# Kernel tuning notes

Measured on AMD Instinct MI355X. Metric: run time of the kernel, lower is better.

The kernel has to match this reference:

```python
import jax, jax.numpy as jnp
import numpy as np

B, U, D, N, O = 128, 16, 256, 1024, 256
RES_CONN, IN_CONN, BIAS_P = 0.2, 0.2, 0.5


def _fixed_bernoulli(rng, heads, rows, cols, conn):
    # each column has exactly nb = int(conn*rows) ones (as in the torch code)
    nb = max(1, int(conn * rows))
    r = rng.random((heads, rows, cols))
    thr = np.sort(r, axis=1)[:, nb - 1:nb, :]
    return (r <= thr).astype(np.float32)


def setup_inputs() -> dict:
    rng = np.random.default_rng(0)
    # recurrent weights: normal * fixed-bernoulli mask, normalized by spectral radius
    W = rng.normal(size=(U, N, N)).astype(np.float32) * _fixed_bernoulli(rng, U, N, N, RES_CONN)
    sr0 = np.abs(np.linalg.eigvals(W.astype(np.float64))).max(axis=-1).astype(np.float32).reshape(U, 1, 1)
    W = W / sr0
    Win = _fixed_bernoulli(rng, U, D, N, IN_CONN)
    bias = (rng.random((U, 1, N)) < BIAS_P).astype(np.float32)
    Wout = rng.normal(size=(U, N, O)).astype(np.float32)
    adaptive_lr = rng.random((U, D, 1)).astype(np.float32)
    sr = rng.random((U, 1, 1)).astype(np.float32)
    temperature = np.ones((1,), np.float32)
    X = rng.normal(size=(B, U, D)).astype(np.float32)
    state = rng.normal(size=(B, U, N)).astype(np.float32)
    arrs = dict(X=X, state=state, W=W, Win=Win, bias=bias, Wout=Wout,
                sr=sr, adaptive_lr=adaptive_lr, temperature=temperature)
    return {k: jnp.asarray(v) for k, v in arrs.items()}


def reference(X, state, W, Win, bias, Wout, sr, adaptive_lr, temperature):
    # X: [B,U,D] -> [B,U,1,D]; state: [B,U,N] -> [B,U,1,N]
    x = X[:, :, None, :]
    s = state[:, :, None, :]
    # adaptive per-unit learning rate: softmax over the units axis
    lr = jax.nn.softmax(jnp.einsum('buid,udk->buik', x, adaptive_lr) / temperature, axis=1)  # [B,U,1,1]
    feed = jnp.einsum('buid,udn->buin', x, Win)            # [B,U,1,N]
    echo = jnp.einsum('buin,unm->buim', s, W * sr) + bias  # [B,U,1,N]
    new_state = (1.0 - lr) * s + lr * jnp.tanh(feed + echo)
    output = jnp.einsum('buin,uno->buio', new_state, Wout)  # [B,U,1,O]
    return new_state[:, :, 0, :], output[:, :, 0, :]
```

## Files before the change

kernel.cpp:

```cpp
#include <hip/hip_runtime.h>
#include <math.h>

#define Bsz 128
#define Usz 16
#define Dsz 256
#define Nsz 1024
#define Osz 256

typedef __attribute__((ext_vector_type(4))) float f32x4;
typedef __attribute__((ext_vector_type(8))) short bf16x8;
typedef __attribute__((ext_vector_type(4))) unsigned int u32x4;

union cell_u { u32x4 u; bf16x8 b; };

struct F8 { f32x4 lo, hi; };

__device__ __forceinline__ unsigned int fbits(float f) {
    union { float f; unsigned int u; } v; v.f = f; return v.u;
}
__device__ __forceinline__ unsigned int pk(float lo, float hi) {
    return __builtin_amdgcn_perm(fbits(hi), fbits(lo), 0x07060302u);
}
__device__ __forceinline__ bf16x8 pkF8(F8 f, float s) {
    f.lo *= s; f.hi *= s;
    cell_u r;
    r.u[0] = pk(f.lo[0], f.lo[1]); r.u[1] = pk(f.lo[2], f.lo[3]);
    r.u[2] = pk(f.hi[0], f.hi[1]); r.u[3] = pk(f.hi[2], f.hi[3]);
    return r.b;
}
__device__ __forceinline__ F8 ld8c(const float* p) {
    F8 r; r.lo = *(const f32x4*)p; r.hi = *(const f32x4*)(p + 4); return r;
}
__device__ __forceinline__ F8 ld8s(const float* p, int str) {
    F8 r;
    r.lo[0] = p[0];              r.lo[1] = p[(size_t)str];
    r.lo[2] = p[2 * (size_t)str]; r.lo[3] = p[3 * (size_t)str];
    r.hi[0] = p[4 * (size_t)str]; r.hi[1] = p[5 * (size_t)str];
    r.hi[2] = p[6 * (size_t)str]; r.hi[3] = p[7 * (size_t)str];
    return r;
}

__global__ __launch_bounds__(256)
void lr_kernel(const float* __restrict__ X, const float* __restrict__ alr,
               const float* __restrict__ temp, float* __restrict__ lr)
{
    const int b = blockIdx.x;
    const int t = threadIdx.x;
    const int u = t >> 4;
    const int l = t & 15;
    const float* xp = X + ((size_t)b * Usz + u) * Dsz;
    const float* ap = alr + (size_t)u * Dsz;
    float s = 0.f;
    for (int d = l; d < Dsz; d += 16) s += xp[d] * ap[d];
    s += __shfl_down(s, 8, 16);
    s += __shfl_down(s, 4, 16);
    s += __shfl_down(s, 2, 16);
    s += __shfl_down(s, 1, 16);
    __shared__ float logits[16];
    if (l == 0) logits[u] = s;
    __syncthreads();
    if (t < 16) {
        const float T = temp[0];
        float m = -1e30f;
        #pragma unroll
        for (int i = 0; i < 16; i++) m = fmaxf(m, logits[i] / T);
        float sum = 0.f;
        #pragma unroll
        for (int i = 0; i < 16; i++) sum += expf(logits[i] / T - m);
        lr[(size_t)b * Usz + t] = expf(logits[t] / T - m) / sum;
    }
}

struct Step { F8 a0, a1, b0, b1; };

__global__ __launch_bounds__(256)
void state_mfma(const float* __restrict__ X, const float* __restrict__ state,
                const float* __restrict__ W, const float* __restrict__ Win,
                const float* __restrict__ bias, const float* __restrict__ sr,
                const float* __restrict__ lr, float* __restrict__ out0)
{
    const int id = blockIdx.x;
    const int u  = id & 15;
    const int nt = (id >> 4) & 15;
    const int mt = id >> 8;

    const int tid  = threadIdx.x;
    const int wave = tid >> 6, lane = tid & 63;
    const int l16  = lane & 15, kgl = lane >> 4;
    const int wm = wave & 1, wn = wave >> 1;

    const int row0 = mt * 64 + wm * 32 + l16;
    const int col0 = nt * 64 + wn * 32 + l16;

    const float sru = sr[u];

    const float* Ax0 = X + ((size_t)row0 * Usz + u) * Dsz;
    const float* Ax1 = X + ((size_t)(row0 + 16) * Usz + u) * Dsz;
    const float* Ae0 = state + ((size_t)row0 * Usz + u) * Nsz;
    const float* Ae1 = state + ((size_t)(row0 + 16) * Usz + u) * Nsz;
    const float* Bf  = Win + (size_t)u * Dsz * Nsz + col0;
    const float* Be  = W   + (size_t)u * Nsz * Nsz + col0;

    f32x4 acc[2][2] = {};

    auto ldS = [&](int s) -> Step {
        const int kb = s * 32 + kgl * 8;
        Step st;
        if (kb < Dsz) {
            st.a0 = ld8c(Ax0 + kb);
            st.a1 = ld8c(Ax1 + kb);
            const float* pb = Bf + (size_t)kb * Nsz;
            st.b0 = ld8s(pb, Nsz);
            st.b1 = ld8s(pb + 16, Nsz);
        } else {
            const int kk = kb - Dsz;
            st.a0 = ld8c(Ae0 + kk);
            st.a1 = ld8c(Ae1 + kk);
            const float* pb = Be + (size_t)kk * Nsz;
            st.b0 = ld8s(pb, Nsz);
            st.b1 = ld8s(pb + 16, Nsz);
        }
        return st;
    };
    auto compute = [&](Step st, int s) {
        const float asc = (s < 8) ? 1.f : sru;
        const bf16x8 af0 = pkF8(st.a0, asc), af1 = pkF8(st.a1, asc);
        const bf16x8 bf0 = pkF8(st.b0, 1.f), bf1 = pkF8(st.b1, 1.f);
        acc[0][0] = __builtin_amdgcn_mfma_f32_16x16x32_bf16(af0, bf0, acc[0][0], 0, 0, 0);
        acc[0][1] = __builtin_amdgcn_mfma_f32_16x16x32_bf16(af0, bf1, acc[0][1], 0, 0, 0);
        acc[1][0] = __builtin_amdgcn_mfma_f32_16x16x32_bf16(af1, bf0, acc[1][0], 0, 0, 0);
        acc[1][1] = __builtin_amdgcn_mfma_f32_16x16x32_bf16(af1, bf1, acc[1][1], 0, 0, 0);
    };

    Step sa = ldS(0);
    for (int s = 0; s < 40; s += 2) {
        Step sb = ldS(s + 1);
        compute(sa, s);
        if (s + 2 < 40) sa = ldS(s + 2);
        compute(sb, s + 1);
    }

    #pragma unroll
    for (int ni = 0; ni < 2; ni++) {
        const int gcol = nt * 64 + wn * 32 + ni * 16 + l16;
        const float bi = bias[u * Nsz + gcol];
        #pragma unroll
        for (int mi = 0; mi < 2; mi++) {
            #pragma unroll
            for (int rg = 0; rg < 4; rg++) {
                const int grow = mt * 64 + wm * 32 + mi * 16 + kgl * 4 + rg;
                const size_t idx = ((size_t)grow * Usz + u) * Nsz + gcol;
                const float th = tanhf(acc[mi][ni][rg] + bi);
                const float sv = state[idx];
                const float lv = lr[grow * Usz + u];
                out0[idx] = (1.f - lv) * sv + lv * th;
            }
        }
    }
}

__global__ __launch_bounds__(256)
void out_mfma(const float* __restrict__ ns, const float* __restrict__ Wout,
              float* __restrict__ out1)
{
    const int w  = blockIdx.x * 4 + (threadIdx.x >> 6);
    const int u  = w & 15;
    const int ot = (w >> 4) & 15;
    const int mtw = w >> 8;

    const int lane = threadIdx.x & 63;
    const int l16  = lane & 15, kgl = lane >> 4;

    const float* Ap = ns + ((size_t)(mtw * 16 + l16) * Usz + u) * Nsz;
    const float* Bp = Wout + (size_t)u * Nsz * Osz + ot * 16 + l16;

    f32x4 acc = {};

    struct Step2 { F8 a, b; };
    auto ldS = [&](int s) -> Step2 {
        const int kb = s * 32 + kgl * 8;
        Step2 st;
        st.a = ld8c(Ap + kb);
        st.b = ld8s(Bp + (size_t)kb * Osz, Osz);
        return st;
    };
    auto compute = [&](Step2 st) {
        const bf16x8 af = pkF8(st.a, 1.f);
        const bf16x8 bf = pkF8(st.b, 1.f);
        acc = __builtin_amdgcn_mfma_f32_16x16x32_bf16(af, bf, acc, 0, 0, 0);
    };

    Step2 sa = ldS(0);
    for (int s = 0; s < 32; s += 2) {
        Step2 sb = ldS(s + 1);
        compute(sa);
        if (s + 2 < 32) sa = ldS(s + 2);
        compute(sb);
    }

    const int gcol = ot * 16 + l16;
    #pragma unroll
    for (int rg = 0; rg < 4; rg++) {
        const int grow = mtw * 16 + kgl * 4 + rg;
        out1[((size_t)grow * Usz + u) * Osz + gcol] = acc[rg];
    }
}

extern "C" void kernel_launch(void* const* d_in, const int* in_sizes, int n_in,
                              void* d_out, int out_size, void* d_ws, size_t ws_size,
                              hipStream_t stream)
{
    (void)in_sizes; (void)n_in; (void)out_size; (void)ws_size;
    const float* X     = (const float*)d_in[0];
    const float* state = (const float*)d_in[1];
    const float* W     = (const float*)d_in[2];
    const float* Win   = (const float*)d_in[3];
    const float* bias  = (const float*)d_in[4];
    const float* Wout  = (const float*)d_in[5];
    const float* sr    = (const float*)d_in[6];
    const float* alr   = (const float*)d_in[7];
    const float* temp  = (const float*)d_in[8];

    float* out0 = (float*)d_out;
    float* out1 = out0 + (size_t)Bsz * Usz * Nsz;
    float* lr   = (float*)d_ws;

    lr_kernel<<<Bsz, 256, 0, stream>>>(X, alr, temp, lr);
    state_mfma<<<512, 256, 0, stream>>>(X, state, W, Win, bias, sr, lr, out0);
    out_mfma<<<512, 256, 0, stream>>>(out0, Wout, out1);
}
```

Measured before the change: 216.7 us.

## Split-K both GEMMs across four slices with separate reduction kernels

Both batched GEMMs are split along K into four slices. Each slice writes partial sums to a workspace, and separate reduce kernels add the partials and apply bias, tanh and the leaky update (or just the sum for the output GEMM). This raises the grid from 512 to 2048 blocks so more CUs stay busy, at the cost of extra global traffic for partials and two more launches. The manual software-pipelined prefetch was also removed, and the old path is kept as a fallback when the workspace is too small.

```diff
diff --git a/kernel.cpp b/kernel.cpp
--- a/kernel.cpp
+++ b/kernel.cpp
@@ -33,7 +33,7 @@
 }
 __device__ __forceinline__ F8 ld8s(const float* p, int str) {
     F8 r;
-    r.lo[0] = p[0];              r.lo[1] = p[(size_t)str];
+    r.lo[0] = p[0];               r.lo[1] = p[(size_t)str];
     r.lo[2] = p[2 * (size_t)str]; r.lo[3] = p[3 * (size_t)str];
     r.hi[0] = p[4 * (size_t)str]; r.hi[1] = p[5 * (size_t)str];
     r.hi[2] = p[6 * (size_t)str]; r.hi[3] = p[7 * (size_t)str];
@@ -71,18 +71,16 @@
     }
 }
 
-struct Step { F8 a0, a1, b0, b1; };
-
-__global__ __launch_bounds__(256)
-void state_mfma(const float* __restrict__ X, const float* __restrict__ state,
-                const float* __restrict__ W, const float* __restrict__ Win,
-                const float* __restrict__ bias, const float* __restrict__ sr,
-                const float* __restrict__ lr, float* __restrict__ out0)
+__global__ __launch_bounds__(256)
+void state_split(const float* __restrict__ X, const float* __restrict__ state,
+                 const float* __restrict__ W, const float* __restrict__ Win,
+                 const float* __restrict__ sr, float* __restrict__ part)
 {
     const int id = blockIdx.x;
     const int u  = id & 15;
     const int nt = (id >> 4) & 15;
-    const int mt = id >> 8;
+    const int mt = (id >> 8) & 1;
+    const int ks = id >> 9;
 
     const int tid  = threadIdx.x;
     const int wave = tid >> 6, lane = tid & 63;
@@ -91,6 +89,7 @@
 
     const int row0 = mt * 64 + wm * 32 + l16;
     const int col0 = nt * 64 + wn * 32 + l16;
+    const int k0   = ks * 320;
 
     const float sru = sr[u];
 
@@ -103,43 +102,180 @@
 
     f32x4 acc[2][2] = {};
 
-    auto ldS = [&](int s) -> Step {
-        const int kb = s * 32 + kgl * 8;
-        Step st;
+    for (int s = 0; s < 10; ++s) {
+        const int kb = k0 + s * 32 + kgl * 8;
+        F8 a0, a1, b0, b1;
         if (kb < Dsz) {
-            st.a0 = ld8c(Ax0 + kb);
-            st.a1 = ld8c(Ax1 + kb);
+            a0 = ld8c(Ax0 + kb);
+            a1 = ld8c(Ax1 + kb);
             const float* pb = Bf + (size_t)kb * Nsz;
-            st.b0 = ld8s(pb, Nsz);
-            st.b1 = ld8s(pb + 16, Nsz);
+            b0 = ld8s(pb, Nsz);
+            b1 = ld8s(pb + 16, Nsz);
         } else {
             const int kk = kb - Dsz;
-            st.a0 = ld8c(Ae0 + kk);
-            st.a1 = ld8c(Ae1 + kk);
+            a0 = ld8c(Ae0 + kk);
+            a1 = ld8c(Ae1 + kk);
             const float* pb = Be + (size_t)kk * Nsz;
-            st.b0 = ld8s(pb, Nsz);
-            st.b1 = ld8s(pb + 16, Nsz);
+            b0 = ld8s(pb, Nsz);
+            b1 = ld8s(pb + 16, Nsz);
         }
-        return st;
-    };
-    auto compute = [&](Step st, int s) {
-        const float asc = (s < 8) ? 1.f : sru;
-        const bf16x8 af0 = pkF8(st.a0, asc), af1 = pkF8(st.a1, asc);
-        const bf16x8 bf0 = pkF8(st.b0, 1.f), bf1 = pkF8(st.b1, 1.f);
+        const float asc = (k0 + s * 32 < Dsz) ? 1.f : sru;
+        const bf16x8 af0 = pkF8(a0, asc), af1 = pkF8(a1, asc);
+        const bf16x8 bf0 = pkF8(b0, 1.f), bf1 = pkF8(b1, 1.f);
         acc[0][0] = __builtin_amdgcn_mfma_f32_16x16x32_bf16(af0, bf0, acc[0][0], 0, 0, 0);
         acc[0][1] = __builtin_amdgcn_mfma_f32_16x16x32_bf16(af0, bf1, acc[0][1], 0, 0, 0);
         acc[1][0] = __builtin_amdgcn_mfma_f32_16x16x32_bf16(af1, bf0, acc[1][0], 0, 0, 0);
         acc[1][1] = __builtin_amdgcn_mfma_f32_16x16x32_bf16(af1, bf1, acc[1][1], 0, 0, 0);
-    };
-
-    Step sa = ldS(0);
-    for (int s = 0; s < 40; s += 2) {
-        Step sb = ldS(s + 1);
-        compute(sa, s);
-        if (s + 2 < 40) sa = ldS(s + 2);
-        compute(sb, s + 1);
-    }
-
+    }
+
+    float* base = part + ((size_t)ks * 16 + u) * 128 * 1024;
+    #pragma unroll
+    for (int ni = 0; ni < 2; ni++) {
+        const int gcol = nt * 64 + wn * 32 + ni * 16 + l16;
+        #pragma unroll
+        for (int mi = 0; mi < 2; mi++) {
+            #pragma unroll
+            for (int rg = 0; rg < 4; rg++) {
+                const int grow = mt * 64 + wm * 32 + mi * 16 + kgl * 4 + rg;
+                base[(size_t)grow * 1024 + gcol] = acc[mi][ni][rg];
+            }
+        }
+    }
+}
+
+__global__ __launch_bounds__(256)
+void state_reduce(const float* __restrict__ part, const float* __restrict__ state,
+                  const float* __restrict__ bias, const float* __restrict__ lr,
+                  float* __restrict__ out0)
+{
+    const size_t i = (size_t)blockIdx.x * 256 + threadIdx.x;
+    const size_t base = i * 4;
+    const int m = (int)(base >> 14);
+    const int u = (int)((base >> 10) & 15);
+    const int n = (int)(base & 1023);
+
+    const size_t pb = ((size_t)u * 128 + m) * 1024 + n;
+    const size_t slab = (size_t)16 * 128 * 1024;
+    f32x4 s = *(const f32x4*)(part + pb);
+    s += *(const f32x4*)(part + pb + slab);
+    s += *(const f32x4*)(part + pb + 2 * slab);
+    s += *(const f32x4*)(part + pb + 3 * slab);
+
+    const f32x4 bi = *(const f32x4*)(bias + (size_t)u * Nsz + n);
+    const f32x4 sv = *(const f32x4*)(state + base);
+    const float lv = lr[m * Usz + u];
+    f32x4 o;
+    o[0] = (1.f - lv) * sv[0] + lv * tanhf(s[0] + bi[0]);
+    o[1] = (1.f - lv) * sv[1] + lv * tanhf(s[1] + bi[1]);
+    o[2] = (1.f - lv) * sv[2] + lv * tanhf(s[2] + bi[2]);
+    o[3] = (1.f - lv) * sv[3] + lv * tanhf(s[3] + bi[3]);
+    *(f32x4*)(out0 + base) = o;
+}
+
+__global__ __launch_bounds__(256)
+void out_split(const float* __restrict__ ns, const float* __restrict__ Wout,
+               float* __restrict__ part)
+{
+    const int id = blockIdx.x;
+    const int u    = id & 15;
+    const int ot   = (id >> 4) & 15;
+    const int mseg = (id >> 8) & 1;
+    const int ks   = id >> 9;
+
+    const int wave = threadIdx.x >> 6, lane = threadIdx.x & 63;
+    const int l16  = lane & 15, kgl = lane >> 4;
+    const int mtw  = mseg * 4 + wave;
+    const int k0   = ks * 256;
+
+    const float* Ap = ns + ((size_t)(mtw * 16 + l16) * Usz + u) * Nsz + k0;
+    const float* Bp = Wout + (size_t)u * Nsz * Osz + (size_t)k0 * Osz + ot * 16 + l16;
+
+    f32x4 acc = {};
+    for (int s = 0; s < 8; ++s) {
+        const int kb = s * 32 + kgl * 8;
+        const F8 a = ld8c(Ap + kb);
+        const F8 b = ld8s(Bp + (size_t)kb * Osz, Osz);
+        acc = __builtin_amdgcn_mfma_f32_16x16x32_bf16(pkF8(a, 1.f), pkF8(b, 1.f), acc, 0, 0, 0);
+    }
+
+    float* base = part + ((size_t)ks * 16 + u) * 128 * 256;
+    const int gcol = ot * 16 + l16;
+    #pragma unroll
+    for (int rg = 0; rg < 4; rg++) {
+        const int grow = mtw * 16 + kgl * 4 + rg;
+        base[(size_t)grow * 256 + gcol] = acc[rg];
+    }
+}
+
+__global__ __launch_bounds__(256)
+void out_reduce(const float* __restrict__ part, float* __restrict__ out1)
+{
+    const size_t i = (size_t)blockIdx.x * 256 + threadIdx.x;
+    const size_t base = i * 4;
+    const int m = (int)(base >> 12);
+    const int u = (int)((base >> 8) & 15);
+    const int o = (int)(base & 255);
+
+    const size_t pb = ((size_t)u * 128 + m) * 256 + o;
+    const size_t slab = (size_t)16 * 128 * 256;
+    f32x4 s = *(const f32x4*)(part + pb);
+    s += *(const f32x4*)(part + pb + slab);
+    s += *(const f32x4*)(part + pb + 2 * slab);
+    s += *(const f32x4*)(part + pb + 3 * slab);
+    *(f32x4*)(out1 + base) = s;
+}
+
+struct Step { F8 a0, a1, b0, b1; };
+
+__global__ __launch_bounds__(256)
+void state_mfma(const float* __restrict__ X, const float* __restrict__ state,
+                const float* __restrict__ W, const float* __restrict__ Win,
+                const float* __restrict__ bias, const float* __restrict__ sr,
+                const float* __restrict__ lr, float* __restrict__ out0)
+{
+    const int id = blockIdx.x;
+    const int u  = id & 15;
+    const int nt = (id >> 4) & 15;
+    const int mt = id >> 8;
+
+    const int tid  = threadIdx.x;
+    const int wave = tid >> 6, lane = tid & 63;
+    const int l16  = lane & 15, kgl = lane >> 4;
+    const int wm = wave & 1, wn = wave >> 1;
+
+    const int row0 = mt * 64 + wm * 32 + l16;
+    const int col0 = nt * 64 + wn * 32 + l16;
+    const float sru = sr[u];
+
+    const float* Ax0 = X + ((size_t)row0 * Usz + u) * Dsz;
+    const float* Ax1 = X + ((size_t)(row0 + 16) * Usz + u) * Dsz;
+    const float* Ae0 = state + ((size_t)row0 * Usz + u) * Nsz;
+    const float* Ae1 = state + ((size_t)(row0 + 16) * Usz + u) * Nsz;
+    const float* Bf  = Win + (size_t)u * Dsz * Nsz + col0;
+    const float* Be  = W   + (size_t)u * Nsz * Nsz + col0;
+
+    f32x4 acc[2][2] = {};
+    for (int s = 0; s < 40; ++s) {
+        const int kb = s * 32 + kgl * 8;
+        F8 a0, a1, b0, b1;
+        if (kb < Dsz) {
+            a0 = ld8c(Ax0 + kb); a1 = ld8c(Ax1 + kb);
+            const float* pb = Bf + (size_t)kb * Nsz;
+            b0 = ld8s(pb, Nsz); b1 = ld8s(pb + 16, Nsz);
+        } else {
+            const int kk = kb - Dsz;
+            a0 = ld8c(Ae0 + kk); a1 = ld8c(Ae1 + kk);
+            const float* pb = Be + (size_t)kk * Nsz;
+            b0 = ld8s(pb, Nsz); b1 = ld8s(pb + 16, Nsz);
+        }
+        const float asc = (s < 8) ? 1.f : sru;
+        const bf16x8 af0 = pkF8(a0, asc), af1 = pkF8(a1, asc);
+        const bf16x8 bf0 = pkF8(b0, 1.f), bf1 = pkF8(b1, 1.f);
+        acc[0][0] = __builtin_amdgcn_mfma_f32_16x16x32_bf16(af0, bf0, acc[0][0], 0, 0, 0);
+        acc[0][1] = __builtin_amdgcn_mfma_f32_16x16x32_bf16(af0, bf1, acc[0][1], 0, 0, 0);
+        acc[1][0] = __builtin_amdgcn_mfma_f32_16x16x32_bf16(af1, bf0, acc[1][0], 0, 0, 0);
+        acc[1][1] = __builtin_amdgcn_mfma_f32_16x16x32_bf16(af1, bf1, acc[1][1], 0, 0, 0);
+    }
     #pragma unroll
     for (int ni = 0; ni < 2; ni++) {
         const int gcol = nt * 64 + wn * 32 + ni * 16 + l16;
@@ -151,9 +287,7 @@
                 const int grow = mt * 64 + wm * 32 + mi * 16 + kgl * 4 + rg;
                 const size_t idx = ((size_t)grow * Usz + u) * Nsz + gcol;
                 const float th = tanhf(acc[mi][ni][rg] + bi);
-                const float sv = state[idx];
-                const float lv = lr[grow * Usz + u];
-                out0[idx] = (1.f - lv) * sv + lv * th;
+                out0[idx] = (1.f - lr[grow * Usz + u]) * state[idx] + lr[grow * Usz + u] * th;
             }
         }
     }
@@ -175,29 +309,12 @@
     const float* Bp = Wout + (size_t)u * Nsz * Osz + ot * 16 + l16;
 
     f32x4 acc = {};
-
-    struct Step2 { F8 a, b; };
-    auto ldS = [&](int s) -> Step2 {
+    for (int s = 0; s < 32; ++s) {
         const int kb = s * 32 + kgl * 8;
-        Step2 st;
-        st.a = ld8c(Ap + kb);
-        st.b = ld8s(Bp + (size_t)kb * Osz, Osz);
-        return st;
-    };
-    auto compute = [&](Step2 st) {
-        const bf16x8 af = pkF8(st.a, 1.f);
-        const bf16x8 bf = pkF8(st.b, 1.f);
-        acc = __builtin_amdgcn_mfma_f32_16x16x32_bf16(af, bf, acc, 0, 0, 0);
-    };
-
-    Step2 sa = ldS(0);
-    for (int s = 0; s < 32; s += 2) {
-        Step2 sb = ldS(s + 1);
-        compute(sa);
-        if (s + 2 < 32) sa = ldS(s + 2);
-        compute(sb);
-    }
-
+        const F8 a = ld8c(Ap + kb);
+        const F8 b = ld8s(Bp + (size_t)kb * Osz, Osz);
+        acc = __builtin_amdgcn_mfma_f32_16x16x32_bf16(pkF8(a, 1.f), pkF8(b, 1.f), acc, 0, 0, 0);
+    }
     const int gcol = ot * 16 + l16;
     #pragma unroll
     for (int rg = 0; rg < 4; rg++) {
@@ -210,7 +327,7 @@
                               void* d_out, int out_size, void* d_ws, size_t ws_size,
                               hipStream_t stream)
 {
-    (void)in_sizes; (void)n_in; (void)out_size; (void)ws_size;
+    (void)in_sizes; (void)n_in; (void)out_size;
     const float* X     = (const float*)d_in[0];
     const float* state = (const float*)d_in[1];
     const float* W     = (const float*)d_in[2];
@@ -225,7 +342,22 @@
     float* out1 = out0 + (size_t)Bsz * Usz * Nsz;
     float* lr   = (float*)d_ws;
 
+    const size_t p1_off = 8192;
+    const size_t p1_bytes = (size_t)4 * 16 * 128 * 1024 * 4;
+    const size_t p2_off = p1_off + p1_bytes;
+    const size_t p2_bytes = (size_t)4 * 16 * 128 * 256 * 4;
+
     lr_kernel<<<Bsz, 256, 0, stream>>>(X, alr, temp, lr);
-    state_mfma<<<512, 256, 0, stream>>>(X, state, W, Win, bias, sr, lr, out0);
-    out_mfma<<<512, 256, 0, stream>>>(out0, Wout, out1);
-}
+
+    if (ws_size >= p2_off + p2_bytes) {
+        float* p1 = (float*)((char*)d_ws + p1_off);
+        float* p2 = (float*)((char*)d_ws + p2_off);
+        state_split<<<2048, 256, 0, stream>>>(X, state, W, Win, sr, p1);
+        state_reduce<<<2048, 256, 0, stream>>>(p1, state, bias, lr, out0);
+        out_split<<<2048, 256, 0, stream>>>(out0, Wout, p2);
+        out_reduce<<<512, 256, 0, stream>>>(p2, out1);
+    } else {
+        state_mfma<<<512, 256, 0, stream>>>(X, state, W, Win, bias, sr, lr, out0);
+        out_mfma<<<512, 256, 0, stream>>>(out0, Wout, out1);
+    }
+}
```

New measurement: 227.1 us. 1.05x slower.
